# Performance work log

Hardware: AMD Instinct MI355X
Metric: run time of the kernel (lower is better)

The kernel has to match this reference:

```python
import jax, jax.numpy as jnp
import numpy as np

# Poincare ball hyperbolic multi-head attention (hypll-style HMultiheadAttention)
C = 1.0          # ball curvature
SQRT_C = 1.0
EPS = 1e-7
B, S, E, H = 4, 1024, 512, 8
HD = E // H      # head_dim = 64


def _project_to_ball(u, scale=0.5):
    n = jnp.linalg.norm(u, axis=-1, keepdims=True)
    return u * (scale / (1.0 + n))  # guarantees ||x|| < scale < 1/sqrt(C)


def h_linear(x, z, r):
    """Poincare fully-connected layer (Shimizu et al. HNN++), as in hypll HLinear.
    x: [..., n] points in the ball, z: [n, m] weight directions, r: [m] bias."""
    x2 = jnp.sum(x * x, -1, keepdims=True)
    lam = 2.0 / jnp.maximum(1.0 - C * x2, EPS)          # conformal factor lambda_x
    zn = jnp.maximum(jnp.linalg.norm(z, axis=0), EPS)    # [m]
    xz = x @ z                                           # [..., m]
    two_cr = 2.0 * SQRT_C * r
    v = (2.0 * zn / SQRT_C) * jnp.arcsinh(
        SQRT_C * lam * xz / zn * jnp.cosh(two_cr) - (lam - 1.0) * jnp.sinh(two_cr)
    )
    v2 = jnp.sum(v * v, -1, keepdims=True)
    return v / (1.0 + jnp.sqrt(1.0 + C * v2))            # map back into the ball


def _split_heads(x):
    b, s, e = x.shape
    return x.reshape(b, s, H, HD).transpose(0, 2, 1, 3)  # [B,H,S,hd]; matches split(dim=-1)


def _h_attention(q, k, v):
    # similarity = -poincare_dist(q, k), pairwise via the arccosh closed form
    # (avoids materializing a [B,H,Sq,Sk,hd] mobius_add tensor)
    q2 = jnp.sum(q * q, -1)[..., :, None]                # [B,H,Sq,1]
    k2 = jnp.sum(k * k, -1)[..., None, :]                # [B,H,1,Sk]
    qk = jnp.einsum('bhqd,bhkd->bhqk', q, k)
    diff2 = jnp.maximum(q2 + k2 - 2.0 * qk, 0.0)
    denom = jnp.maximum((1.0 - C * q2) * (1.0 - C * k2), EPS)
    arg = 1.0 + 2.0 * C * diff2 / denom
    dist = jnp.arccosh(jnp.maximum(arg, 1.0 + EPS)) / SQRT_C
    w = jax.nn.softmax(-dist, axis=-1)                   # attention_activation
    # attention_midpoint: weighted Mobius gyromidpoint then half scalar-mul
    v2 = jnp.sum(v * v, -1)                              # [B,H,Sk]
    lam = 2.0 / jnp.maximum(1.0 - C * v2, EPS)
    num = jnp.einsum('bhqk,bhkd->bhqd', w * lam[..., None, :], v)
    den = jnp.einsum('bhqk,bhk->bhq', w, lam - 1.0)[..., None]
    m_bar = num / jnp.where(jnp.abs(den) < EPS, EPS, den)
    mn = jnp.maximum(jnp.linalg.norm(m_bar, axis=-1, keepdims=True), EPS)
    t = jnp.minimum(SQRT_C * mn, 1.0 - 1e-6)
    return jnp.tanh(0.5 * jnp.arctanh(t)) * m_bar / (SQRT_C * mn)  # (1/2) mobius-scalar-mul


def setup_inputs() -> dict:
    key = jax.random.key(0)
    ks = jax.random.split(key, 9)
    query = _project_to_ball(jax.random.normal(ks[0], (B, S, E), jnp.float32))
    key_t = _project_to_ball(jax.random.normal(ks[1], (B, S, E), jnp.float32))
    value = _project_to_ball(jax.random.normal(ks[2], (B, S, E), jnp.float32))
    scale = E ** -0.5
    zq = jax.random.normal(ks[3], (E, E), jnp.float32) * scale
    zk = jax.random.normal(ks[4], (E, E), jnp.float32) * scale
    zv = jax.random.normal(ks[5], (E, E), jnp.float32) * scale
    rq = jax.random.normal(ks[6], (E,), jnp.float32) * 0.01
    rk = jax.random.normal(ks[7], (E,), jnp.float32) * 0.01
    rv = jax.random.normal(ks[8], (E,), jnp.float32) * 0.01
    return {"query": query, "key": key_t, "value": value,
            "zq": zq, "rq": rq, "zk": zk, "rk": rk, "zv": zv, "rv": rv}


def reference(query, key, value, zq, rq, zk, rk, zv, rv):
    pq = h_linear(query, zq, rq)
    pk = h_linear(key, zk, rk)
    pv = h_linear(value, zv, rv)
    q, k, v = _split_heads(pq), _split_heads(pk), _split_heads(pv)
    out = _h_attention(q, k, v)                          # [B,H,S,hd]
    return out.transpose(0, 2, 1, 3).reshape(B, S, E)    # manifold.cat over heads
```

## Files before the change

### kernel.cpp

```cpp
#include <hip/hip_runtime.h>
#include <hip/hip_bf16.h>
#include <math.h>

#define EPSf 1e-7f
typedef unsigned short u16;
typedef __attribute__((ext_vector_type(8))) short bf16x8;
typedef __attribute__((ext_vector_type(4))) float f32x4;

__device__ __forceinline__ float bf2f(u16 u) {
  union { unsigned int i; float f; } x; x.i = ((unsigned int)u) << 16; return x.f;
}
__device__ __forceinline__ u16 f2bf(float f) {
  union { float f; unsigned int i; } x; x.f = f;
  unsigned int r = x.i + 0x7fffu + ((x.i >> 16) & 1u);
  return (u16)(r >> 16);
}
__device__ __forceinline__ void gll16(const void* g, void* l) {
  __builtin_amdgcn_global_load_lds((__attribute__((address_space(1))) void*)(g),
                                   (__attribute__((address_space(3))) void*)(l),
                                   16, 0, 0);
}

__global__ __launch_bounds__(256) void prep(
    const float* __restrict__ xq, const float* __restrict__ xk, const float* __restrict__ xv,
    const float* __restrict__ zq, const float* __restrict__ zk, const float* __restrict__ zv,
    u16* __restrict__ Xh, u16* __restrict__ Xl,
    float* __restrict__ Xn, float* __restrict__ Vn,
    u16* __restrict__ ZhT, u16* __restrict__ ZlT, float* __restrict__ Zn) {
  __shared__ float tile[64][68];
  const int t = threadIdx.x;
  if (blockIdx.x < 6144) {
    const int gr = blockIdx.x * 2 + (t >> 7);
    const int mat = gr >> 12, row = gr & 4095;
    const float* X = (mat == 0) ? xq : (mat == 1) ? xk : xv;
    const int f4 = t & 127;
    float4 x = ((const float4*)(X + (size_t)row * 512))[f4];
    u16 h0 = f2bf(x.x), h1 = f2bf(x.y), h2 = f2bf(x.z), h3 = f2bf(x.w);
    u16 l0 = f2bf(x.x - bf2f(h0)), l1 = f2bf(x.y - bf2f(h1));
    u16 l2 = f2bf(x.z - bf2f(h2)), l3 = f2bf(x.w - bf2f(h3));
    ((ushort4*)(Xh + (size_t)gr * 512))[f4] = make_ushort4(h0, h1, h2, h3);
    ((ushort4*)(Xl + (size_t)gr * 512))[f4] = make_ushort4(l0, l1, l2, l3);
    float a = fmaf(x.x, x.x, fmaf(x.y, x.y, fmaf(x.z, x.z, x.w * x.w)));
    a += __shfl_xor(a, 1);  a += __shfl_xor(a, 2);  a += __shfl_xor(a, 4);
    a += __shfl_xor(a, 8);  a += __shfl_xor(a, 16); a += __shfl_xor(a, 32);
    if ((t & 63) == 0) tile[0][t >> 6] = a;
    __syncthreads();
    if (t == 0)   { Xn[gr] = tile[0][0] + tile[0][1]; Vn[gr] = 0.f; }
    if (t == 128) { Xn[gr] = tile[0][2] + tile[0][3]; Vn[gr] = 0.f; }
  } else {
    const int idx = blockIdx.x - 6144;
    const int mat = idx >> 6;
    const int cg = (idx >> 3) & 7, kt = idx & 7;
    const int c0 = cg * 64;
    const float* Z = (mat == 0) ? zq : (mat == 1) ? zk : zv;
    {
      int kl = t >> 2;
      const float* src = Z + (size_t)(kt * 64 + kl) * 512 + c0 + (t & 3) * 16;
      #pragma unroll
      for (int j = 0; j < 4; ++j) {
        float4 v = *(const float4*)(src + 4 * j);
        *(float4*)&tile[kl][(t & 3) * 16 + 4 * j] = v;
      }
    }
    __syncthreads();
    const int cl = t >> 2, kg4 = t & 3;
    const size_t zo = (size_t)mat * 512 * 512;
    float csum = 0.f;
    #pragma unroll
    for (int jj = 0; jj < 4; ++jj) {
      u16 hb[4], lb[4];
      #pragma unroll
      for (int qq = 0; qq < 4; ++qq) {
        float zval = tile[kg4 * 16 + jj * 4 + qq][cl];
        csum = fmaf(zval, zval, csum);
        u16 hh = f2bf(zval);
        hb[qq] = hh;
        lb[qq] = f2bf(zval - bf2f(hh));
      }
      size_t o = zo + (size_t)(c0 + cl) * 512 + kt * 64 + kg4 * 16 + jj * 4;
      *(ushort4*)(ZhT + o) = make_ushort4(hb[0], hb[1], hb[2], hb[3]);
      *(ushort4*)(ZlT + o) = make_ushort4(lb[0], lb[1], lb[2], lb[3]);
    }
    csum += __shfl_xor(csum, 1);
    csum += __shfl_xor(csum, 2);
    if (kg4 == 0) atomicAdd(&Zn[mat * 512 + c0 + cl], csum);
  }
}

__global__ __launch_bounds__(256) void proj_gemm(
    const u16* __restrict__ Xh, const u16* __restrict__ Xl,
    const u16* __restrict__ ZhT, const u16* __restrict__ ZlT,
    const float* __restrict__ Xn, const float* __restrict__ Zn,
    const float* __restrict__ rq, const float* __restrict__ rk, const float* __restrict__ rv,
    float* __restrict__ Vtmp, float* __restrict__ Vn) {
  const int m0 = blockIdx.x * 64;
  const int n0 = blockIdx.y * 128;
  const int mat = blockIdx.z;
  const size_t xoff = (size_t)mat * 4096 * 512;
  const size_t zoff = (size_t)mat * 512 * 512;
  const int t = threadIdx.x, wv = t >> 6, lane = t & 63;
  const int l15 = lane & 15, quad = lane >> 4;
  const int wm = wv >> 1, wn = wv & 1;

  __shared__ __align__(16) u16 SM[12288];
  __shared__ float lams[64], lam1s[64], wmxs[128], wmys[128], wmzs[128];

  if (t < 64) {
    float x2 = Xn[mat * 4096 + m0 + t];
    float lam = 2.f / fmaxf(1.f - x2, EPSf);
    lams[t] = lam; lam1s[t] = lam - 1.f;
  }
  if (t < 128) {
    float zn = fmaxf(sqrtf(Zn[mat * 512 + n0 + t]), EPSf);
    const float* R = (mat == 0) ? rq : (mat == 1) ? rk : rv;
    float tr = 2.f * R[n0 + t];
    float e = expf(tr), ei = 1.f / e;
    wmxs[t] = 0.5f * (e + ei) / zn;
    wmys[t] = 0.5f * (e - ei);
    wmzs[t] = 2.f * zn;
  }

  f32x4 acc[2][4];
  #pragma unroll
  for (int i = 0; i < 2; ++i)
    #pragma unroll
    for (int j = 0; j < 4; ++j) acc[i][j] = (f32x4){0.f, 0.f, 0.f, 0.f};

  const u16* gs[6];
  u16* ld[6];
  #pragma unroll
  for (int ci = 0; ci < 6; ++ci) {
    int c = wv + 4 * ci;
    const u16* arr; int row0, lo;
    if (c < 4)       { arr = Xh + xoff;  row0 = m0 + 16 * c;        lo = c * 512; }
    else if (c < 8)  { arr = Xl + xoff;  row0 = m0 + 16 * (c - 4);  lo = 2048 + (c - 4) * 512; }
    else if (c < 16) { arr = ZhT + zoff; row0 = n0 + 16 * (c - 8);  lo = 4096 + (c - 8) * 512; }
    else             { arr = ZlT + zoff; row0 = n0 + 16 * (c - 16); lo = 8192 + (c - 16) * 512; }
    gs[ci] = arr + (size_t)(row0 + (lane >> 2)) * 512 + (lane & 3) * 8;
    ld[ci] = SM + lo;
  }

  for (int k0 = 0; k0 < 512; k0 += 32) {
    __syncthreads();
    #pragma unroll
    for (int ci = 0; ci < 6; ++ci) gll16(gs[ci] + k0, ld[ci]);
    __syncthreads();
    bf16x8 ah[2], al[2], bh_[4], bl_[4];
    #pragma unroll
    for (int i = 0; i < 2; ++i) {
      int ra = wm * 32 + i * 16 + l15;
      ah[i] = *(const bf16x8*)&SM[ra * 32 + quad * 8];
      al[i] = *(const bf16x8*)&SM[2048 + ra * 32 + quad * 8];
    }
    #pragma unroll
    for (int j = 0; j < 4; ++j) {
      int rb = wn * 64 + j * 16 + l15;
      bh_[j] = *(const bf16x8*)&SM[4096 + rb * 32 + quad * 8];
      bl_[j] = *(const bf16x8*)&SM[8192 + rb * 32 + quad * 8];
    }
    #pragma unroll
    for (int i = 0; i < 2; ++i)
      #pragma unroll
      for (int j = 0; j < 4; ++j) {
        acc[i][j] = __builtin_amdgcn_mfma_f32_16x16x32_bf16(ah[i], bh_[j], acc[i][j], 0, 0, 0);
        acc[i][j] = __builtin_amdgcn_mfma_f32_16x16x32_bf16(ah[i], bl_[j], acc[i][j], 0, 0, 0);
        acc[i][j] = __builtin_amdgcn_mfma_f32_16x16x32_bf16(al[i], bh_[j], acc[i][j], 0, 0, 0);
      }
  }

  #pragma unroll
  for (int i = 0; i < 2; ++i) {
    float rsum[4] = {0.f, 0.f, 0.f, 0.f};
    #pragma unroll
    for (int j = 0; j < 4; ++j) {
      int nl = wn * 64 + j * 16 + l15;
      float wx = wmxs[nl], wy = wmys[nl], wz = wmzs[nl];
      #pragma unroll
      for (int r = 0; r < 4; ++r) {
        int ml = wm * 32 + i * 16 + quad * 4 + r;
        float tt = lams[ml] * acc[i][j][r] * wx - lam1s[ml] * wy;
        float v = wz * logf(tt + sqrtf(fmaf(tt, tt, 1.f)));
        Vtmp[xoff + (size_t)(m0 + ml) * 512 + (n0 + nl)] = v;
        rsum[r] = fmaf(v, v, rsum[r]);
      }
    }
    #pragma unroll
    for (int r = 0; r < 4; ++r) {
      rsum[r] += __shfl_xor(rsum[r], 1);
      rsum[r] += __shfl_xor(rsum[r], 2);
      rsum[r] += __shfl_xor(rsum[r], 4);
      rsum[r] += __shfl_xor(rsum[r], 8);
    }
    if (l15 == 0) {
      #pragma unroll
      for (int r = 0; r < 4; ++r)
        atomicAdd(&Vn[mat * 4096 + m0 + wm * 32 + i * 16 + quad * 4 + r], rsum[r]);
    }
  }
}

__global__ __launch_bounds__(256) void pack(
    const float* __restrict__ Vtmp, const float* __restrict__ Vn,
    u16* __restrict__ Qh, u16* __restrict__ Kh, u16* __restrict__ VTb,
    float* __restrict__ q2a, float* __restrict__ aqa, float4* __restrict__ ksc) {
  __shared__ u16 tile[64][72];
  __shared__ float lams[64];
  const int t = threadIdx.x;
  if (blockIdx.x < 256) {
    const int mat = blockIdx.x >> 7;
    const int b   = (blockIdx.x >> 5) & 3;
    const int h   = (blockIdx.x >> 2) & 7;
    const int sq  = blockIdx.x & 3;
    const int s8 = t >> 3, d8 = t & 7;
    u16* outbase = (mat ? Kh : Qh) + (size_t)(b * 8 + h) * 65536;
    #pragma unroll
    for (int p = 0; p < 8; ++p) {
      const int s = sq * 256 + p * 32 + s8;
      const size_t gr = (size_t)mat * 4096 + b * 1024 + s;
      const float sc = 1.f / (1.f + sqrtf(1.f + Vn[gr]));
      const float* src = Vtmp + gr * 512 + h * 64 + d8 * 8;
      float4 xa = *(const float4*)src;
      float4 xb = *(const float4*)(src + 4);
      u16 u0 = f2bf(xa.x * sc), u1 = f2bf(xa.y * sc), u2 = f2bf(xa.z * sc), u3 = f2bf(xa.w * sc);
      u16 u4 = f2bf(xb.x * sc), u5 = f2bf(xb.y * sc), u6 = f2bf(xb.z * sc), u7 = f2bf(xb.w * sc);
      uint4 pkd;
      pkd.x = (unsigned)u0 | ((unsigned)u1 << 16);
      pkd.y = (unsigned)u2 | ((unsigned)u3 << 16);
      pkd.z = (unsigned)u4 | ((unsigned)u5 << 16);
      pkd.w = (unsigned)u6 | ((unsigned)u7 << 16);
      *(uint4*)(outbase + (size_t)s * 64 + d8 * 8) = pkd;
      float f0 = bf2f(u0), f1 = bf2f(u1), f2 = bf2f(u2), f3 = bf2f(u3);
      float f4 = bf2f(u4), f5 = bf2f(u5), f6 = bf2f(u6), f7 = bf2f(u7);
      float nrm = f0*f0 + f1*f1 + f2*f2 + f3*f3 + f4*f4 + f5*f5 + f6*f6 + f7*f7;
      nrm += __shfl_xor(nrm, 1);
      nrm += __shfl_xor(nrm, 2);
      nrm += __shfl_xor(nrm, 4);
      if (d8 == 0) {
        const size_t so = (size_t)(b * 8 + h) * 1024 + s;
        if (mat == 0) { q2a[so] = nrm; aqa[so] = 1.f / fmaxf(1.f - nrm, EPSf); }
        else {
          *(float2*)&ksc[so] = make_float2(nrm, 2.f / fmaxf(1.f - nrm, EPSf));
        }
      }
    }
  } else {
    const int idx = blockIdx.x - 256;
    const int bh = idx >> 4, st = idx & 15;
    const int b = bh >> 3, h = bh & 7;
    {
      const int s = t >> 2, dg = t & 3;
      const size_t gr = (size_t)2 * 4096 + b * 1024 + st * 64 + s;
      const float sc = 1.f / (1.f + sqrtf(1.f + Vn[gr]));
      const float* src = Vtmp + gr * 512 + h * 64 + dg * 16;
      float nrm = 0.f;
      #pragma unroll
      for (int j = 0; j < 4; ++j) {
        float4 x = *(const float4*)(src + 4 * j);
        u16 u0 = f2bf(x.x * sc), u1 = f2bf(x.y * sc), u2 = f2bf(x.z * sc), u3 = f2bf(x.w * sc);
        *(ushort4*)&tile[s][dg * 16 + 4 * j] = make_ushort4(u0, u1, u2, u3);
        float f0 = bf2f(u0), f1 = bf2f(u1), f2 = bf2f(u2), f3 = bf2f(u3);
        nrm += f0 * f0 + f1 * f1 + f2 * f2 + f3 * f3;
      }
      nrm += __shfl_xor(nrm, 1);
      nrm += __shfl_xor(nrm, 2);
      if (dg == 0) {
        float lam = 2.f / fmaxf(1.f - nrm, EPSf);
        lams[s] = lam;
        ((float*)&ksc[(size_t)bh * 1024 + st * 64 + s])[3] = lam - 1.f;
      }
    }
    __syncthreads();
    const int d = t >> 2, sg = t & 3;
    u16 ob[16];
    #pragma unroll
    for (int j = 0; j < 16; ++j) {
      int ss = sg * 16 + j;
      ob[j] = f2bf(bf2f(tile[ss][d]) * lams[ss]);
    }
    u16* dst = VTb + ((size_t)bh * 64 + d) * 1024 + st * 64 + sg * 16;
    #pragma unroll
    for (int j = 0; j < 4; ++j)
      *(ushort4*)(dst + 4 * j) = make_ushort4(ob[4 * j], ob[4 * j + 1], ob[4 * j + 2], ob[4 * j + 3]);
  }
}

__global__ __launch_bounds__(256, 3) void attn(
    const u16* __restrict__ Qh, const u16* __restrict__ Kh, const u16* __restrict__ VTb,
    const float* __restrict__ q2a, const float* __restrict__ aqa,
    const float4* __restrict__ ksc, float* __restrict__ out) {
  const int bh = blockIdx.x;
  const int b = bh >> 3, h = bh & 7;
  const int q0 = blockIdx.y * 32;
  const int t = threadIdx.x, wv = t >> 6, lane = t & 63;
  const int l15 = lane & 15, quad = lane >> 4;
  const int kq = wv;

  __shared__ __align__(16) u16 Ws[4][32 * 72];
  __shared__ float k2s[4][64], cks[4][64], l1s[4][64];
  __shared__ __align__(16) float nums[2][32][68];
  __shared__ float dens[2][32];

  const size_t qkoff = (size_t)bh * 65536;

  bf16x8 qf[2][2];
  float q2r[2], aqr[2];
  #pragma unroll
  for (int qs = 0; qs < 2; ++qs) {
    int qrow = q0 + qs * 16 + l15;
    const u16* qp = Qh + qkoff + (size_t)qrow * 64 + quad * 8;
    qf[qs][0] = *(const bf16x8*)qp;
    qf[qs][1] = *(const bf16x8*)(qp + 32);
    q2r[qs] = q2a[bh * 1024 + qrow];
    aqr[qs] = aqa[bh * 1024 + qrow];
  }

  f32x4 num[2][4];
  #pragma unroll
  for (int qs = 0; qs < 2; ++qs)
    #pragma unroll
    for (int tm = 0; tm < 4; ++tm) num[qs][tm] = (f32x4){0.f, 0.f, 0.f, 0.f};
  float denp[2] = {0.f, 0.f};

  bf16x8 kcur[8];
  #pragma unroll
  for (int tn = 0; tn < 4; ++tn)
    #pragma unroll
    for (int ks = 0; ks < 2; ++ks)
      kcur[tn * 2 + ks] = *(const bf16x8*)(Kh + qkoff +
          (size_t)(kq * 64 + tn * 16 + l15) * 64 + ks * 32 + quad * 8);
  float4 scur = ksc[bh * 1024 + kq * 64 + lane];

  #pragma unroll 1
  for (int i = 0; i < 4; ++i) {
    const int ktc = kq + 4 * i;
    const int kti = (i < 3) ? ktc + 4 : ktc;
    bf16x8 knxt[8];
    #pragma unroll
    for (int tn = 0; tn < 4; ++tn)
      #pragma unroll
      for (int ks = 0; ks < 2; ++ks)
        knxt[tn * 2 + ks] = *(const bf16x8*)(Kh + qkoff +
            (size_t)(kti * 64 + tn * 16 + l15) * 64 + ks * 32 + quad * 8);
    float4 snxt = ksc[bh * 1024 + kti * 64 + lane];
    k2s[wv][lane] = scur.x;
    cks[wv][lane] = scur.y;
    l1s[wv][lane] = scur.w;

    #pragma unroll
    for (int tn = 0; tn < 4; ++tn) {
      const float4 k2v = *(const float4*)&k2s[wv][tn * 16 + quad * 4];
      const float4 ckv = *(const float4*)&cks[wv][tn * 16 + quad * 4];
      const float4 l1v = *(const float4*)&l1s[wv][tn * 16 + quad * 4];
      #pragma unroll
      for (int qs = 0; qs < 2; ++qs) {
        f32x4 s = (f32x4){0.f, 0.f, 0.f, 0.f};
        s = __builtin_amdgcn_mfma_f32_16x16x32_bf16(kcur[tn * 2 + 0], qf[qs][0], s, 0, 0, 0);
        s = __builtin_amdgcn_mfma_f32_16x16x32_bf16(kcur[tn * 2 + 1], qf[qs][1], s, 0, 0, 0);
        unsigned up[2];
        #pragma unroll
        for (int pr = 0; pr < 2; ++pr) {
          float w2[2];
          #pragma unroll
          for (int e = 0; e < 2; ++e) {
            const int r = pr * 2 + e;
            float d2 = fmaxf(fmaf(-2.f, s[r], q2r[qs] + ((const float*)&k2v)[r]), 0.f);
            float u = fmaxf(d2 * ((const float*)&ckv)[r] * aqr[qs], EPSf);
            w2[e] = (1.f + u) - sqrtf(fmaf(u, u, u + u));
          }
          union { __hip_bfloat162 h2; unsigned u; } cv;
          cv.h2 = __float22bfloat162_rn(make_float2(w2[0], w2[1]));
          up[pr] = cv.u;
          float wlo = __uint_as_float(cv.u << 16);
          float whi = __uint_as_float(cv.u & 0xffff0000u);
          denp[qs] = fmaf(wlo, ((const float*)&l1v)[pr * 2 + 0], denp[qs]);
          denp[qs] = fmaf(whi, ((const float*)&l1v)[pr * 2 + 1], denp[qs]);
        }
        *(uint2*)&Ws[wv][(qs * 16 + l15) * 72 + tn * 16 + quad * 4] = make_uint2(up[0], up[1]);
      }
    }
    #pragma unroll
    for (int ks = 0; ks < 2; ++ks) {
      bf16x8 vfk[4];
      #pragma unroll
      for (int tm = 0; tm < 4; ++tm)
        vfk[tm] = *(const bf16x8*)(VTb + qkoff +
            (size_t)(tm * 16 + l15) * 1024 + ktc * 64 + ks * 32 + quad * 8);
      #pragma unroll
      for (int qs = 0; qs < 2; ++qs) {
        const bf16x8 wf = *(const bf16x8*)&Ws[wv][(qs * 16 + l15) * 72 + ks * 32 + quad * 8];
        #pragma unroll
        for (int tm = 0; tm < 4; ++tm)
          num[qs][tm] = __builtin_amdgcn_mfma_f32_16x16x32_bf16(
              vfk[tm], wf, num[qs][tm], 0, 0, 0);
      }
    }
    #pragma unroll
    for (int j = 0; j < 8; ++j) kcur[j] = knxt[j];
    scur = snxt;
  }

  #pragma unroll
  for (int qs = 0; qs < 2; ++qs) {
    denp[qs] += __shfl_xor(denp[qs], 16);
    denp[qs] += __shfl_xor(denp[qs], 32);
  }

  if (wv & 1) {
    const int buf = wv >> 1;
    #pragma unroll
    for (int qs = 0; qs < 2; ++qs) {
      #pragma unroll
      for (int tm = 0; tm < 4; ++tm)
        *(float4*)&nums[buf][qs * 16 + l15][tm * 16 + quad * 4] =
            make_float4(num[qs][tm][0], num[qs][tm][1], num[qs][tm][2], num[qs][tm][3]);
      if (quad == 0) dens[buf][qs * 16 + l15] = denp[qs];
    }
  }
  __syncthreads();
  if (!(wv & 1)) {
    const int buf = wv >> 1;
    #pragma unroll
    for (int qs = 0; qs < 2; ++qs) {
      #pragma unroll
      for (int tm = 0; tm < 4; ++tm) {
        float4 o = *(const float4*)&nums[buf][qs * 16 + l15][tm * 16 + quad * 4];
        num[qs][tm][0] += o.x; num[qs][tm][1] += o.y;
        num[qs][tm][2] += o.z; num[qs][tm][3] += o.w;
      }
      denp[qs] += dens[buf][qs * 16 + l15];
    }
  }
  if (wv == 2) {
    #pragma unroll
    for (int qs = 0; qs < 2; ++qs) {
      #pragma unroll
      for (int tm = 0; tm < 4; ++tm)
        *(float4*)&nums[1][qs * 16 + l15][tm * 16 + quad * 4] =
            make_float4(num[qs][tm][0], num[qs][tm][1], num[qs][tm][2], num[qs][tm][3]);
      if (quad == 0) dens[1][qs * 16 + l15] = denp[qs];
    }
  }
  __syncthreads();
  if (wv == 0) {
    #pragma unroll
    for (int qs = 0; qs < 2; ++qs) {
      #pragma unroll
      for (int tm = 0; tm < 4; ++tm) {
        float4 o = *(const float4*)&nums[1][qs * 16 + l15][tm * 16 + quad * 4];
        num[qs][tm][0] += o.x; num[qs][tm][1] += o.y;
        num[qs][tm][2] += o.z; num[qs][tm][3] += o.w;
      }
      float den = denp[qs] + dens[1][qs * 16 + l15];
      den = (fabsf(den) < EPSf) ? EPSf : den;
      float inv = 1.f / den;
      float mv[4][4];
      float p = 0.f;
      #pragma unroll
      for (int tm = 0; tm < 4; ++tm) {
        mv[tm][0] = num[qs][tm][0] * inv;
        mv[tm][1] = num[qs][tm][1] * inv;
        mv[tm][2] = num[qs][tm][2] * inv;
        mv[tm][3] = num[qs][tm][3] * inv;
        p = fmaf(mv[tm][0], mv[tm][0], p); p = fmaf(mv[tm][1], mv[tm][1], p);
        p = fmaf(mv[tm][2], mv[tm][2], p); p = fmaf(mv[tm][3], mv[tm][3], p);
      }
      p += __shfl_xor(p, 16);
      p += __shfl_xor(p, 32);
      float mn = sqrtf(p);
      float mnc = fmaxf(mn, EPSf);
      float tt2 = fminf(mnc, 1.f - 1e-6f);
      float scale = tt2 / ((1.f + sqrtf(fmaxf(1.f - tt2 * tt2, 0.f))) * mnc);
      const size_t qg = (size_t)b * 1024 + q0 + qs * 16 + l15;
      #pragma unroll
      for (int tm = 0; tm < 4; ++tm) {
        float4 o = make_float4(mv[tm][0] * scale, mv[tm][1] * scale,
                               mv[tm][2] * scale, mv[tm][3] * scale);
        *(float4*)(out + qg * 512 + h * 64 + tm * 16 + quad * 4) = o;
      }
    }
  }
}

extern "C" void kernel_launch(void* const* d_in, const int* in_sizes, int n_in,
                              void* d_out, int out_size, void* d_ws, size_t ws_size,
                              hipStream_t stream) {
  (void)in_sizes; (void)n_in; (void)out_size; (void)ws_size;
  const float* q  = (const float*)d_in[0];
  const float* k  = (const float*)d_in[1];
  const float* v  = (const float*)d_in[2];
  const float* zq = (const float*)d_in[3];
  const float* rq = (const float*)d_in[4];
  const float* zk = (const float*)d_in[5];
  const float* rk = (const float*)d_in[6];
  const float* zv = (const float*)d_in[7];
  const float* rv = (const float*)d_in[8];

  unsigned char* ws = (unsigned char*)d_ws;
  u16*   Xh   = (u16*)(ws + 0);
  u16*   Xl   = (u16*)(ws + 12582912);
  u16*   ZhT  = (u16*)(ws + 25165824);
  u16*   ZlT  = (u16*)(ws + 26738688);
  float* Vtmp = (float*)(ws + 28311552);
  float* Xn   = (float*)(ws + 53477376);
  float* Vn   = (float*)(ws + 53526528);
  float* Zn   = (float*)(ws + 53575680);
  u16*   Qh   = (u16*)(ws + 0);
  u16*   Kh   = (u16*)(ws + 4194304);
  u16*   VTb  = (u16*)(ws + 8388608);
  float* q2a  = (float*)(ws + 12582912);
  float* aqa  = (float*)(ws + 12713984);
  float4* ksc = (float4*)(ws + 12845056);

  hipMemsetAsync(Zn, 0, 6144, stream);
  prep<<<6336, 256, 0, stream>>>(q, k, v, zq, zk, zv, Xh, Xl, Xn, Vn, ZhT, ZlT, Zn);
  proj_gemm<<<dim3(64, 4, 3), 256, 0, stream>>>(Xh, Xl, ZhT, ZlT, Xn, Zn, rq, rk, rv, Vtmp, Vn);
  pack<<<768, 256, 0, stream>>>(Vtmp, Vn, Qh, Kh, VTb, q2a, aqa, ksc);
  attn<<<dim3(32, 32), 256, 0, stream>>>(Qh, Kh, VTb, q2a, aqa, ksc, (float*)d_out);
}
```

Before: 172.9 us.

## Halve attention query tile to 16 rows and raise occupancy

The attention kernel now processes 16 query rows per block instead of 32, doubling the grid to 32x64 blocks and raising launch bounds to 5 blocks per CU. The K register double-buffering prefetch is removed. The reduction scratch now aliases the per-wave W tile in shared memory, with an extra barrier before reuse. This cuts registers and LDS per block to allow more waves in flight. In exchange, every K and V tile is loaded twice as often across the grid, and loads are no longer overlapped with compute.

```diff
diff --git a/kernel.cpp b/kernel.cpp
--- a/kernel.cpp
+++ b/kernel.cpp
@@ -284,99 +284,80 @@
   }
 }
 
-__global__ __launch_bounds__(256, 3) void attn(
+__global__ __launch_bounds__(256, 5) void attn(
     const u16* __restrict__ Qh, const u16* __restrict__ Kh, const u16* __restrict__ VTb,
     const float* __restrict__ q2a, const float* __restrict__ aqa,
     const float4* __restrict__ ksc, float* __restrict__ out) {
   const int bh = blockIdx.x;
   const int b = bh >> 3, h = bh & 7;
-  const int q0 = blockIdx.y * 32;
+  const int q0 = blockIdx.y * 16;
   const int t = threadIdx.x, wv = t >> 6, lane = t & 63;
   const int l15 = lane & 15, quad = lane >> 4;
   const int kq = wv;
 
-  __shared__ __align__(16) u16 Ws[4][32 * 72];
+  __shared__ __align__(16) u16 WsAll[4 * 16 * 72];
   __shared__ float k2s[4][64], cks[4][64], l1s[4][64];
-  __shared__ __align__(16) float nums[2][32][68];
-  __shared__ float dens[2][32];
+  __shared__ float dens[2][16];
+  u16* Ws = WsAll + wv * (16 * 72);
+  float* numsf = (float*)WsAll;
 
   const size_t qkoff = (size_t)bh * 65536;
 
-  bf16x8 qf[2][2];
-  float q2r[2], aqr[2];
+  const int qrow = q0 + l15;
+  const u16* qp = Qh + qkoff + (size_t)qrow * 64 + quad * 8;
+  const bf16x8 qf0 = *(const bf16x8*)qp;
+  const bf16x8 qf1 = *(const bf16x8*)(qp + 32);
+  const float q2r = q2a[bh * 1024 + qrow];
+  const float aqr = aqa[bh * 1024 + qrow];
+
+  f32x4 num[4];
   #pragma unroll
-  for (int qs = 0; qs < 2; ++qs) {
-    int qrow = q0 + qs * 16 + l15;
-    const u16* qp = Qh + qkoff + (size_t)qrow * 64 + quad * 8;
-    qf[qs][0] = *(const bf16x8*)qp;
-    qf[qs][1] = *(const bf16x8*)(qp + 32);
-    q2r[qs] = q2a[bh * 1024 + qrow];
-    aqr[qs] = aqa[bh * 1024 + qrow];
-  }
-
-  f32x4 num[2][4];
-  #pragma unroll
-  for (int qs = 0; qs < 2; ++qs)
-    #pragma unroll
-    for (int tm = 0; tm < 4; ++tm) num[qs][tm] = (f32x4){0.f, 0.f, 0.f, 0.f};
-  float denp[2] = {0.f, 0.f};
-
-  bf16x8 kcur[8];
-  #pragma unroll
-  for (int tn = 0; tn < 4; ++tn)
-    #pragma unroll
-    for (int ks = 0; ks < 2; ++ks)
-      kcur[tn * 2 + ks] = *(const bf16x8*)(Kh + qkoff +
-          (size_t)(kq * 64 + tn * 16 + l15) * 64 + ks * 32 + quad * 8);
-  float4 scur = ksc[bh * 1024 + kq * 64 + lane];
+  for (int tm = 0; tm < 4; ++tm) num[tm] = (f32x4){0.f, 0.f, 0.f, 0.f};
+  float denp = 0.f;
 
   #pragma unroll 1
   for (int i = 0; i < 4; ++i) {
     const int ktc = kq + 4 * i;
-    const int kti = (i < 3) ? ktc + 4 : ktc;
-    bf16x8 knxt[8];
-    #pragma unroll
-    for (int tn = 0; tn < 4; ++tn)
-      #pragma unroll
-      for (int ks = 0; ks < 2; ++ks)
-        knxt[tn * 2 + ks] = *(const bf16x8*)(Kh + qkoff +
-            (size_t)(kti * 64 + tn * 16 + l15) * 64 + ks * 32 + quad * 8);
-    float4 snxt = ksc[bh * 1024 + kti * 64 + lane];
+    float4 scur = ksc[bh * 1024 + ktc * 64 + lane];
     k2s[wv][lane] = scur.x;
     cks[wv][lane] = scur.y;
     l1s[wv][lane] = scur.w;
+    bf16x8 kcur[8];
+    #pragma unroll
+    for (int tn = 0; tn < 4; ++tn)
+      #pragma unroll
+      for (int ks = 0; ks < 2; ++ks)
+        kcur[tn * 2 + ks] = *(const bf16x8*)(Kh + qkoff +
+            (size_t)(ktc * 64 + tn * 16 + l15) * 64 + ks * 32 + quad * 8);
 
     #pragma unroll
     for (int tn = 0; tn < 4; ++tn) {
       const float4 k2v = *(const float4*)&k2s[wv][tn * 16 + quad * 4];
       const float4 ckv = *(const float4*)&cks[wv][tn * 16 + quad * 4];
       const float4 l1v = *(const float4*)&l1s[wv][tn * 16 + quad * 4];
-      #pragma unroll
-      for (int qs = 0; qs < 2; ++qs) {
-        f32x4 s = (f32x4){0.f, 0.f, 0.f, 0.f};
-        s = __builtin_amdgcn_mfma_f32_16x16x32_bf16(kcur[tn * 2 + 0], qf[qs][0], s, 0, 0, 0);
-        s = __builtin_amdgcn_mfma_f32_16x16x32_bf16(kcur[tn * 2 + 1], qf[qs][1], s, 0, 0, 0);
-        unsigned up[2];
+      f32x4 s = (f32x4){0.f, 0.f, 0.f, 0.f};
+      s = __builtin_amdgcn_mfma_f32_16x16x32_bf16(kcur[tn * 2 + 0], qf0, s, 0, 0, 0);
+      s = __builtin_amdgcn_mfma_f32_16x16x32_bf16(kcur[tn * 2 + 1], qf1, s, 0, 0, 0);
+      unsigned up[2];
+      #pragma unroll
+      for (int pr = 0; pr < 2; ++pr) {
+        float w2[2];
         #pragma unroll
-        for (int pr = 0; pr < 2; ++pr) {
-          float w2[2];
-          #pragma unroll
-          for (int e = 0; e < 2; ++e) {
-            const int r = pr * 2 + e;
-            float d2 = fmaxf(fmaf(-2.f, s[r], q2r[qs] + ((const float*)&k2v)[r]), 0.f);
-            float u = fmaxf(d2 * ((const float*)&ckv)[r] * aqr[qs], EPSf);
-            w2[e] = (1.f + u) - sqrtf(fmaf(u, u, u + u));
-          }
-          union { __hip_bfloat162 h2; unsigned u; } cv;
-          cv.h2 = __float22bfloat162_rn(make_float2(w2[0], w2[1]));
-          up[pr] = cv.u;
-          float wlo = __uint_as_float(cv.u << 16);
-          float whi = __uint_as_float(cv.u & 0xffff0000u);
-          denp[qs] = fmaf(wlo, ((const float*)&l1v)[pr * 2 + 0], denp[qs]);
-          denp[qs] = fmaf(whi, ((const float*)&l1v)[pr * 2 + 1], denp[qs]);
+        for (int e = 0; e < 2; ++e) {
+          const int r = pr * 2 + e;
+          float d2 = fmaxf(fmaf(-2.f, s[r], q2r + ((const float*)&k2v)[r]), 0.f);
+          float u = fmaxf(d2 * ((const float*)&ckv)[r] * aqr, EPSf);
+          w2[e] = (1.f + u) - sqrtf(fmaf(u, u, u + u));
         }
-        *(uint2*)&Ws[wv][(qs * 16 + l15) * 72 + tn * 16 + quad * 4] = make_uint2(up[0], up[1]);
-      }
+        union { __hip_bfloat162 h2; unsigned u; } cv;
+        cv.h2 = __float22bfloat162_rn(make_float2(w2[0], w2[1]));
+        up[pr] = cv.u;
+        float wlo = __uint_as_float(cv.u << 16);
+        float whi = __uint_as_float(cv.u & 0xffff0000u);
+        denp = fmaf(wlo, ((const float*)&l1v)[pr * 2 + 0], denp);
+        denp = fmaf(whi, ((const float*)&l1v)[pr * 2 + 1], denp);
+      }
+      *(uint2*)&Ws[l15 * 72 + tn * 16 + quad * 4] = make_uint2(up[0], up[1]);
     }
     #pragma unroll
     for (int ks = 0; ks < 2; ++ks) {
@@ -385,98 +366,76 @@
       for (int tm = 0; tm < 4; ++tm)
         vfk[tm] = *(const bf16x8*)(VTb + qkoff +
             (size_t)(tm * 16 + l15) * 1024 + ktc * 64 + ks * 32 + quad * 8);
-      #pragma unroll
-      for (int qs = 0; qs < 2; ++qs) {
-        const bf16x8 wf = *(const bf16x8*)&Ws[wv][(qs * 16 + l15) * 72 + ks * 32 + quad * 8];
-        #pragma unroll
-        for (int tm = 0; tm < 4; ++tm)
-          num[qs][tm] = __builtin_amdgcn_mfma_f32_16x16x32_bf16(
-              vfk[tm], wf, num[qs][tm], 0, 0, 0);
-      }
-    }
-    #pragma unroll
-    for (int j = 0; j < 8; ++j) kcur[j] = knxt[j];
-    scur = snxt;
-  }
-
-  #pragma unroll
-  for (int qs = 0; qs < 2; ++qs) {
-    denp[qs] += __shfl_xor(denp[qs], 16);
-    denp[qs] += __shfl_xor(denp[qs], 32);
-  }
+      const bf16x8 wf = *(const bf16x8*)&Ws[l15 * 72 + ks * 32 + quad * 8];
+      #pragma unroll
+      for (int tm = 0; tm < 4; ++tm)
+        num[tm] = __builtin_amdgcn_mfma_f32_16x16x32_bf16(vfk[tm], wf, num[tm], 0, 0, 0);
+    }
+  }
+
+  denp += __shfl_xor(denp, 16);
+  denp += __shfl_xor(denp, 32);
+
+  __syncthreads();
 
   if (wv & 1) {
     const int buf = wv >> 1;
     #pragma unroll
-    for (int qs = 0; qs < 2; ++qs) {
-      #pragma unroll
-      for (int tm = 0; tm < 4; ++tm)
-        *(float4*)&nums[buf][qs * 16 + l15][tm * 16 + quad * 4] =
-            make_float4(num[qs][tm][0], num[qs][tm][1], num[qs][tm][2], num[qs][tm][3]);
-      if (quad == 0) dens[buf][qs * 16 + l15] = denp[qs];
-    }
+    for (int tm = 0; tm < 4; ++tm)
+      *(float4*)&numsf[(buf * 16 + l15) * 68 + tm * 16 + quad * 4] =
+          make_float4(num[tm][0], num[tm][1], num[tm][2], num[tm][3]);
+    if (quad == 0) dens[buf][l15] = denp;
   }
   __syncthreads();
   if (!(wv & 1)) {
     const int buf = wv >> 1;
     #pragma unroll
-    for (int qs = 0; qs < 2; ++qs) {
-      #pragma unroll
-      for (int tm = 0; tm < 4; ++tm) {
-        float4 o = *(const float4*)&nums[buf][qs * 16 + l15][tm * 16 + quad * 4];
-        num[qs][tm][0] += o.x; num[qs][tm][1] += o.y;
-        num[qs][tm][2] += o.z; num[qs][tm][3] += o.w;
-      }
-      denp[qs] += dens[buf][qs * 16 + l15];
-    }
+    for (int tm = 0; tm < 4; ++tm) {
+      float4 o = *(const float4*)&numsf[(buf * 16 + l15) * 68 + tm * 16 + quad * 4];
+      num[tm][0] += o.x; num[tm][1] += o.y; num[tm][2] += o.z; num[tm][3] += o.w;
+    }
+    denp += dens[buf][l15];
   }
   if (wv == 2) {
     #pragma unroll
-    for (int qs = 0; qs < 2; ++qs) {
-      #pragma unroll
-      for (int tm = 0; tm < 4; ++tm)
-        *(float4*)&nums[1][qs * 16 + l15][tm * 16 + quad * 4] =
-            make_float4(num[qs][tm][0], num[qs][tm][1], num[qs][tm][2], num[qs][tm][3]);
-      if (quad == 0) dens[1][qs * 16 + l15] = denp[qs];
-    }
+    for (int tm = 0; tm < 4; ++tm)
+      *(float4*)&numsf[(16 + l15) * 68 + tm * 16 + quad * 4] =
+          make_float4(num[tm][0], num[tm][1], num[tm][2], num[tm][3]);
+    if (quad == 0) dens[1][l15] = denp;
   }
   __syncthreads();
   if (wv == 0) {
     #pragma unroll
-    for (int qs = 0; qs < 2; ++qs) {
-      #pragma unroll
-      for (int tm = 0; tm < 4; ++tm) {
-        float4 o = *(const float4*)&nums[1][qs * 16 + l15][tm * 16 + quad * 4];
-        num[qs][tm][0] += o.x; num[qs][tm][1] += o.y;
-        num[qs][tm][2] += o.z; num[qs][tm][3] += o.w;
-      }
-      float den = denp[qs] + dens[1][qs * 16 + l15];
-      den = (fabsf(den) < EPSf) ? EPSf : den;
-      float inv = 1.f / den;
-      float mv[4][4];
-      float p = 0.f;
-      #pragma unroll
-      for (int tm = 0; tm < 4; ++tm) {
-        mv[tm][0] = num[qs][tm][0] * inv;
-        mv[tm][1] = num[qs][tm][1] * inv;
-        mv[tm][2] = num[qs][tm][2] * inv;
-        mv[tm][3] = num[qs][tm][3] * inv;
-        p = fmaf(mv[tm][0], mv[tm][0], p); p = fmaf(mv[tm][1], mv[tm][1], p);
-        p = fmaf(mv[tm][2], mv[tm][2], p); p = fmaf(mv[tm][3], mv[tm][3], p);
-      }
-      p += __shfl_xor(p, 16);
-      p += __shfl_xor(p, 32);
-      float mn = sqrtf(p);
-      float mnc = fmaxf(mn, EPSf);
-      float tt2 = fminf(mnc, 1.f - 1e-6f);
-      float scale = tt2 / ((1.f + sqrtf(fmaxf(1.f - tt2 * tt2, 0.f))) * mnc);
-      const size_t qg = (size_t)b * 1024 + q0 + qs * 16 + l15;
-      #pragma unroll
-      for (int tm = 0; tm < 4; ++tm) {
-        float4 o = make_float4(mv[tm][0] * scale, mv[tm][1] * scale,
-                               mv[tm][2] * scale, mv[tm][3] * scale);
-        *(float4*)(out + qg * 512 + h * 64 + tm * 16 + quad * 4) = o;
-      }
+    for (int tm = 0; tm < 4; ++tm) {
+      float4 o = *(const float4*)&numsf[(16 + l15) * 68 + tm * 16 + quad * 4];
+      num[tm][0] += o.x; num[tm][1] += o.y; num[tm][2] += o.z; num[tm][3] += o.w;
+    }
+    float den = denp + dens[1][l15];
+    den = (fabsf(den) < EPSf) ? EPSf : den;
+    float inv = 1.f / den;
+    float mv[4][4];
+    float p = 0.f;
+    #pragma unroll
+    for (int tm = 0; tm < 4; ++tm) {
+      mv[tm][0] = num[tm][0] * inv;
+      mv[tm][1] = num[tm][1] * inv;
+      mv[tm][2] = num[tm][2] * inv;
+      mv[tm][3] = num[tm][3] * inv;
+      p = fmaf(mv[tm][0], mv[tm][0], p); p = fmaf(mv[tm][1], mv[tm][1], p);
+      p = fmaf(mv[tm][2], mv[tm][2], p); p = fmaf(mv[tm][3], mv[tm][3], p);
+    }
+    p += __shfl_xor(p, 16);
+    p += __shfl_xor(p, 32);
+    float mn = sqrtf(p);
+    float mnc = fmaxf(mn, EPSf);
+    float tt2 = fminf(mnc, 1.f - 1e-6f);
+    float scale = tt2 / ((1.f + sqrtf(fmaxf(1.f - tt2 * tt2, 0.f))) * mnc);
+    const size_t qg = (size_t)b * 1024 + q0 + l15;
+    #pragma unroll
+    for (int tm = 0; tm < 4; ++tm) {
+      float4 o = make_float4(mv[tm][0] * scale, mv[tm][1] * scale,
+                             mv[tm][2] * scale, mv[tm][3] * scale);
+      *(float4*)(out + qg * 512 + h * 64 + tm * 16 + quad * 4) = o;
     }
   }
 }
@@ -515,5 +474,5 @@
   prep<<<6336, 256, 0, stream>>>(q, k, v, zq, zk, zv, Xh, Xl, Xn, Vn, ZhT, ZlT, Zn);
   proj_gemm<<<dim3(64, 4, 3), 256, 0, stream>>>(Xh, Xl, ZhT, ZlT, Xn, Zn, rq, rk, rv, Vtmp, Vn);
   pack<<<768, 256, 0, stream>>>(Vtmp, Vn, Qh, Kh, VTb, q2a, aqa, ksc);
-  attn<<<dim3(32, 32), 256, 0, stream>>>(Qh, Kh, VTb, q2a, aqa, ksc, (float*)d_out);
-}
+  attn<<<dim3(32, 64), 256, 0, stream>>>(Qh, Kh, VTb, q2a, aqa, ksc, (float*)d_out);
+}
```

After: 195.0 us. +12.8%, slower.
